# Kernel tuning notes

Measured on AMD Instinct MI355X. Metric: run time of the kernel, lower is better.

The kernel has to match this reference:

```python
import jax, jax.numpy as jnp
import numpy as np
from jax import lax

B, C, TX, TY = 16, 192, 512, 2048
SEG = 8192 // 256  # segment_frames = 32 (hop length 256)
NEG_INF = -1e9


def setup_inputs() -> dict:
    key = jax.random.key(0)
    ks = jax.random.split(key, 7)
    z = jax.random.normal(ks[0], (B, C, TY), jnp.float32)
    z_p = jax.random.normal(ks[1], (B, C, TY), jnp.float32)
    m_p = jax.random.normal(ks[2], (B, C, TX), jnp.float32)
    logs_p = 0.1 * jax.random.normal(ks[3], (B, C, TX), jnp.float32)
    x_lengths = jax.random.randint(ks[4], (B,), TX // 2, TX + 1, jnp.int32)
    y_lengths = jax.random.randint(ks[5], (B,), TY // 2, TY + 1, jnp.int32)
    rand_u = jax.random.uniform(ks[6], (B,), jnp.float32)
    return dict(z=z, z_p=z_p, m_p=m_p, logs_p=logs_p,
                x_lengths=x_lengths, y_lengths=y_lengths, rand_u=rand_u)


def neg_cent_fn(z_p, m_p, logs_p):
    # sum_c -0.5 * exp(-2 logs)[c,tx] * (z_p[c,ty] - m_p[c,tx])^2 - sum_c logs[c,tx]
    # expanded (z-m)^2 = z^2 - 2 z m + m^2 -> batched GEMMs (same math as broadcast form)
    s = jnp.exp(-2.0 * logs_p)                                 # [B,C,Tx]
    a = jnp.einsum('bct,bcs->bts', -0.5 * z_p * z_p, s)        # [B,Ty,Tx]
    b = jnp.einsum('bct,bcs->bts', z_p, s * m_p)               # [B,Ty,Tx]
    c = jnp.sum(-0.5 * s * m_p * m_p - logs_p, axis=1)         # [B,Tx]
    return a + b + c[:, None, :]


def maximum_path_single(value, t_x, t_y):
    # Monotonic alignment search DP on value [Ty,Tx], valid region [:t_y,:t_x].
    Ty, Tx = value.shape
    tx = jnp.arange(Tx)

    def fwd(v, row):
        v_shift = jnp.concatenate([jnp.full((1,), NEG_INF, v.dtype), v[:-1]])
        dirn = v_shift > v                      # True: best predecessor is tx-1
        v_new = row + jnp.maximum(v, v_shift)
        v_new = jnp.where(tx < t_x, v_new, NEG_INF)
        v_new = jnp.maximum(v_new, NEG_INF)     # clamp accumulation
        return v_new, dirn

    v0 = jnp.where(tx == 0, 0.0, NEG_INF)
    _, dirs = lax.scan(fwd, v0, value)          # dirs [Ty,Tx] bool

    def bwd(idx, j):
        active = j < t_y
        idx = jnp.where(j == t_y - 1, t_x - 1, idx)
        row = jnp.where(active, jnp.zeros((Tx,), value.dtype).at[idx].set(1.0), 0.0)
        idx = jnp.where(active, idx - dirs[j, idx].astype(idx.dtype), idx)
        return idx, row

    _, path_rev = lax.scan(bwd, jnp.int32(0), jnp.arange(Ty - 1, -1, -1))
    return path_rev[::-1]                       # [Ty,Tx] 0/1 path


def rand_slice_segments(z, y_lengths, rand_u):
    t = z.shape[2]
    safe = jnp.minimum(y_lengths, t)
    ids_max = jnp.maximum(safe - SEG, 0)
    ids = (rand_u * (ids_max.astype(jnp.float32) + 1e-8)).astype(jnp.int32)
    zs = jax.vmap(lambda zi, s: lax.dynamic_slice_in_dim(zi, s, SEG, axis=1))(z, ids)
    valid = (jnp.arange(SEG)[None, None, :] < (safe - ids)[:, None, None])
    return zs * valid.astype(z.dtype), ids


def reference(z, z_p, m_p, logs_p, x_lengths, y_lengths, rand_u):
    neg_cent = neg_cent_fn(z_p, m_p, logs_p)                     # [B,Ty,Tx]
    attn = jax.vmap(maximum_path_single)(neg_cent, x_lengths, y_lengths)
    attn = lax.stop_gradient(attn)                               # torch: no_grad + detach
    m_p_a = jnp.einsum('bts,bcs->bct', attn, m_p)                # [B,C,Ty]
    logs_p_a = jnp.einsum('bts,bcs->bct', attn, logs_p)          # [B,C,Ty]
    z_slice, ids_slice = rand_slice_segments(z, y_lengths, rand_u)
    return z_slice, ids_slice, attn, m_p_a, logs_p_a
```

## Files before the change

kernel.cpp:

```cpp
#include <hip/hip_runtime.h>
#include <stdint.h>

#define B_   16
#define C_   192
#define TX_  512
#define TY_  2048
#define K_   384
#define SEG_ 32
#define NEG_INF_ (-1e9f)


__global__ __launch_bounds__(128) void k_prep(const float* __restrict__ mp,
                                              const float* __restrict__ logsp,
                                              float* __restrict__ Bmat,
                                              float* __restrict__ cterm) {
    int b  = blockIdx.y;
    int tx = blockIdx.x * 128 + threadIdx.x;
    const float* mb = mp    + (size_t)b * C_ * TX_ + tx;
    const float* lb = logsp + (size_t)b * C_ * TX_ + tx;
    float* B0 = Bmat + (size_t)b * K_ * TX_ + tx;
    float acc = 0.f;
    for (int c = 0; c < C_; ++c) {
        float lg = lb[(size_t)c * TX_];
        float m  = mb[(size_t)c * TX_];
        float s  = expf(-2.f * lg);
        B0[(size_t)c * TX_]        = s;
        B0[(size_t)(C_ + c) * TX_] = s * m;
        acc += -0.5f * s * m * m - lg;
    }
    cterm[b * TX_ + tx] = acc;
}

__global__ __launch_bounds__(256) void k_gemm(const float* __restrict__ zp,
                                              const float* __restrict__ Bmat,
                                              const float* __restrict__ cterm,
                                              float* __restrict__ ncout) {
    __shared__ float As[16][128];
    __shared__ float Bs[16][128];
    int b  = blockIdx.z;
    int m0 = blockIdx.y * 128;
    int n0 = blockIdx.x * 128;
    int tid = threadIdx.x;
    int tm = tid >> 4;
    int tn = tid & 15;
    const float* zpb = zp   + (size_t)b * C_ * TY_;
    const float* Bb  = Bmat + (size_t)b * K_ * TX_;

    float acc[8][8];
#pragma unroll
    for (int i = 0; i < 8; ++i)
#pragma unroll
        for (int j = 0; j < 8; ++j) acc[i][j] = 0.f;

    int lrow = tid >> 5;
    int lcol = (tid & 31) << 2;

    for (int k0 = 0; k0 < K_; k0 += 16) {
        int ksrc = (k0 < C_) ? k0 : (k0 - C_);
        const float* Ab = zpb + (size_t)(ksrc + lrow) * TY_ + m0 + lcol;
        float4 z0 = *(const float4*)Ab;
        float4 z1 = *(const float4*)(Ab + (size_t)8 * TY_);
        if (k0 < C_) {
            z0.x = -0.5f * z0.x * z0.x; z0.y = -0.5f * z0.y * z0.y;
            z0.z = -0.5f * z0.z * z0.z; z0.w = -0.5f * z0.w * z0.w;
            z1.x = -0.5f * z1.x * z1.x; z1.y = -0.5f * z1.y * z1.y;
            z1.z = -0.5f * z1.z * z1.z; z1.w = -0.5f * z1.w * z1.w;
        }
        const float* Bp = Bb + (size_t)(k0 + lrow) * TX_ + n0 + lcol;
        float4 w0 = *(const float4*)Bp;
        float4 w1 = *(const float4*)(Bp + (size_t)8 * TX_);

        __syncthreads();
        *(float4*)&As[lrow][lcol]     = z0;
        *(float4*)&As[lrow + 8][lcol] = z1;
        *(float4*)&Bs[lrow][lcol]     = w0;
        *(float4*)&Bs[lrow + 8][lcol] = w1;
        __syncthreads();

#pragma unroll
        for (int kk = 0; kk < 16; ++kk) {
            float4 a0 = *(const float4*)&As[kk][tm * 8];
            float4 a1 = *(const float4*)&As[kk][tm * 8 + 4];
            float4 b0 = *(const float4*)&Bs[kk][tn * 8];
            float4 b1 = *(const float4*)&Bs[kk][tn * 8 + 4];
            float a[8]  = {a0.x, a0.y, a0.z, a0.w, a1.x, a1.y, a1.z, a1.w};
            float bb[8] = {b0.x, b0.y, b0.z, b0.w, b1.x, b1.y, b1.z, b1.w};
#pragma unroll
            for (int i = 0; i < 8; ++i)
#pragma unroll
                for (int j = 0; j < 8; ++j)
                    acc[i][j] = fmaf(a[i], bb[j], acc[i][j]);
        }
    }

    float cadd[8];
#pragma unroll
    for (int j = 0; j < 8; ++j) cadd[j] = cterm[b * TX_ + n0 + tn * 8 + j];

#pragma unroll
    for (int i = 0; i < 8; ++i) {
        int row = m0 + tm * 8 + i;
        float* orow = ncout + ((size_t)b * TY_ + row) * TX_ + n0 + tn * 8;
        float4 o0, o1;
        o0.x = acc[i][0] + cadd[0]; o0.y = acc[i][1] + cadd[1];
        o0.z = acc[i][2] + cadd[2]; o0.w = acc[i][3] + cadd[3];
        o1.x = acc[i][4] + cadd[4]; o1.y = acc[i][5] + cadd[5];
        o1.z = acc[i][6] + cadd[6]; o1.w = acc[i][7] + cadd[7];
        *(float4*)orow       = o0;
        *(float4*)(orow + 4) = o1;
    }
}

#define LOADG(g, P0, P1)                                                     \
    {                                                                        \
        const float* rp = base + (size_t)(g) * 8 * TX_;                      \
        _Pragma("unroll") for (int r = 0; r < 8; ++r) {                      \
            P0[r] = *(const float4*)(rp + (size_t)r * TX_);                  \
            P1[r] = *(const float4*)(rp + (size_t)r * TX_ + 4);              \
        }                                                                    \
    }

#define PROCG(g, P0, P1)                                                     \
    {                                                                        \
        unsigned dw0 = 0u, dw1 = 0u;                                         \
        _Pragma("unroll") for (int r = 0; r < 8; ++r) {                      \
            float rc[8] = {P0[r].x, P0[r].y, P0[r].z, P0[r].w,               \
                           P1[r].x, P1[r].y, P1[r].z, P1[r].w};              \
            float left = __shfl_up(v[7], 1);                                 \
            if (lane == 0) left = NEG_INF_;                                  \
            unsigned by = 0u;                                                \
            _Pragma("unroll") for (int k = 7; k >= 0; --k) {                 \
                float vs = (k == 0) ? left : v[k - 1];                       \
                if (vs > v[k]) by |= (1u << k);                              \
                v[k] = fmaxf(v[k], vs) + rc[k];                              \
            }                                                                \
            if (r < 4) dw0 |= by << (8 * r);                                 \
            else       dw1 |= by << (8 * (r - 4));                           \
        }                                                                    \
        sdirs32[((g) * 2) * 64 + lane]     = dw0;                            \
        sdirs32[((g) * 2 + 1) * 64 + lane] = dw1;                            \
    }

__global__ __launch_bounds__(64, 1) void k_dp(const float* __restrict__ nc,
                                              const int* __restrict__ xl,
                                              const int* __restrict__ yl,
                                              int* __restrict__ path) {
    extern __shared__ unsigned char sdirs[];
    unsigned* sdirs32 = (unsigned*)sdirs;
    int b    = blockIdx.x;
    int lane = threadIdx.x;
    int t_x  = xl[b];
    int t_y  = yl[b]; if (t_y > TY_) t_y = TY_;
    const float* base = nc + (size_t)b * TY_ * TX_ + lane * 8;

    int col0 = lane * 8;
    float v[8];
#pragma unroll
    for (int k = 0; k < 8; ++k) v[k] = (col0 + k == 0) ? 0.f : NEG_INF_;

    float4 c0[8], c1[8], n0[8], n1[8];
    int ng = (t_y + 7) >> 3;

    LOADG(0, c0, c1);
    for (int g = 0; g < ng; g += 2) {
        if (g + 1 < ng) LOADG(g + 1, n0, n1);
        __builtin_amdgcn_sched_barrier(0);
        PROCG(g, c0, c1);
        if (g + 1 < ng) {
            if (g + 2 < ng) LOADG(g + 2, c0, c1);
            __builtin_amdgcn_sched_barrier(0);
            PROCG(g + 1, n0, n1);
        }
    }

    __syncthreads();

    int* pb = path + b * TY_;
    for (int j = t_y + lane; j < TY_; j += 64) pb[j] = -1;

    if (lane == 0) {
        int idx = t_x - 1;
        int j   = t_y - 1;
        while (j >= 0) {
            int n  = (j + 1 < 8) ? (j + 1) : 8;
            int bs = (idx - 7) >> 3; if (bs < 0) bs = 0;
            int b2 = bs + 1;         if (b2 > 63) b2 = 63;
            unsigned lo[8], hi[8];
#pragma unroll
            for (int r = 0; r < 8; ++r) {
                if (r < n) {
                    int jr = j - r;
                    int rb = (jr >> 2) * 256 + (jr & 3);
                    lo[r] = sdirs[rb + bs * 4];
                    hi[r] = sdirs[rb + b2 * 4];
                }
            }
#pragma unroll
            for (int r = 0; r < 8; ++r) {
                if (r < n) {
                    pb[j - r] = idx;
                    int Bi = idx >> 3;
                    unsigned byte = (Bi == bs) ? lo[r] : hi[r];
                    idx -= (int)((byte >> (idx & 7)) & 1u);
                }
            }
            j -= n;
        }
    }
}

__global__ __launch_bounds__(256) void k_attn(const int* __restrict__ path,
                                              float* __restrict__ attn) {
    int i   = blockIdx.x * 256 + threadIdx.x;
    int tx0 = (i & 127) << 2;
    int bty = i >> 7;
    int p   = path[bty];
    float4 o;
    o.x = (p == tx0)     ? 1.f : 0.f;
    o.y = (p == tx0 + 1) ? 1.f : 0.f;
    o.z = (p == tx0 + 2) ? 1.f : 0.f;
    o.w = (p == tx0 + 3) ? 1.f : 0.f;
    ((float4*)attn)[i] = o;
}

__global__ __launch_bounds__(256) void k_proj(const int* __restrict__ path,
                                              const float* __restrict__ mp,
                                              const float* __restrict__ logsp,
                                              float* __restrict__ mpa,
                                              float* __restrict__ logsa) {
    int i   = blockIdx.x * 256 + threadIdx.x;
    int ty0 = (i & 511) << 2;
    int bc  = i >> 9;
    int b   = bc / C_;
    const int4 p4 = *(const int4*)(path + b * TY_ + ty0);
    const float* mrow = mp    + (size_t)bc * TX_;
    const float* lrow = logsp + (size_t)bc * TX_;
    float4 mo, lo;
    mo.x = (p4.x >= 0) ? mrow[p4.x] : 0.f;  lo.x = (p4.x >= 0) ? lrow[p4.x] : 0.f;
    mo.y = (p4.y >= 0) ? mrow[p4.y] : 0.f;  lo.y = (p4.y >= 0) ? lrow[p4.y] : 0.f;
    mo.z = (p4.z >= 0) ? mrow[p4.z] : 0.f;  lo.z = (p4.z >= 0) ? lrow[p4.z] : 0.f;
    mo.w = (p4.w >= 0) ? mrow[p4.w] : 0.f;  lo.w = (p4.w >= 0) ? lrow[p4.w] : 0.f;
    ((float4*)mpa)[i]   = mo;
    ((float4*)logsa)[i] = lo;
}

__global__ __launch_bounds__(256) void k_slice(const float* __restrict__ z,
                                               const int* __restrict__ yl,
                                               const float* __restrict__ ru,
                                               float* __restrict__ zs,
                                               float* __restrict__ oid) {
    int b = blockIdx.x;
    int safe = yl[b]; if (safe > TY_) safe = TY_;
    int idsmax = safe - SEG_; if (idsmax < 0) idsmax = 0;
    int ids = (int)(ru[b] * ((float)idsmax + 1e-8f));
    int lim = safe - ids;
    for (int t = threadIdx.x; t < C_ * SEG_; t += 256) {
        int c = t >> 5, k = t & 31;
        zs[b * C_ * SEG_ + t] =
            (k < lim) ? z[((size_t)b * C_ + c) * TY_ + ids + k] : 0.f;
    }
    if (threadIdx.x == 0) oid[b] = (float)ids;
}

extern "C" void kernel_launch(void* const* d_in, const int* in_sizes, int n_in,
                              void* d_out, int out_size, void* d_ws, size_t ws_size,
                              hipStream_t stream) {
    const float* z     = (const float*)d_in[0];
    const float* zp    = (const float*)d_in[1];
    const float* mp    = (const float*)d_in[2];
    const float* logsp = (const float*)d_in[3];
    const int*   xl    = (const int*)d_in[4];
    const int*   yl    = (const int*)d_in[5];
    const float* ru    = (const float*)d_in[6];

    float* out     = (float*)d_out;
    float* o_zs    = out;
    float* o_ids   = out + 98304;
    float* o_attn  = out + 98320;
    float* o_mpa   = out + 16875536;
    float* o_logsa = out + 23166992;

    float* Bmat  = (float*)d_ws;
    float* cterm = Bmat + (size_t)B_ * K_ * TX_;
    int*   path  = (int*)(cterm + B_ * TX_);

    hipFuncSetAttribute((const void*)k_dp,
                        hipFuncAttributeMaxDynamicSharedMemorySize,
                        TY_ * 64);

    hipLaunchKernelGGL(k_prep, dim3(TX_ / 128, B_), dim3(128), 0, stream,
                       mp, logsp, Bmat, cterm);
    hipLaunchKernelGGL(k_gemm, dim3(TX_ / 128, TY_ / 128, B_), dim3(256), 0, stream,
                       zp, Bmat, cterm, o_attn);
    hipLaunchKernelGGL(k_dp, dim3(B_), dim3(64), TY_ * 64, stream,
                       o_attn, xl, yl, path);
    hipLaunchKernelGGL(k_attn, dim3(B_ * TY_ * TX_ / 4 / 256), dim3(256), 0, stream,
                       path, o_attn);
    hipLaunchKernelGGL(k_proj, dim3(B_ * C_ * TY_ / 4 / 256), dim3(256), 0, stream,
                       path, mp, logsp, o_mpa, o_logsa);
    hipLaunchKernelGGL(k_slice, dim3(B_), dim3(256), 0, stream,
                       z, yl, ru, o_zs, o_ids);
}
```

Baseline: 778.6 us.

## Stream DP rows through LDS with async global_load_lds triple buffering

```diff
diff --git a/kernel.cpp b/kernel.cpp
--- a/kernel.cpp
+++ b/kernel.cpp
@@ -111,21 +111,28 @@
     }
 }
 
-#define LOADG(g, P0, P1)                                                     \
+#define WAITVM8() __builtin_amdgcn_s_waitcnt(3960)
+#define WAITVM0() __builtin_amdgcn_s_waitcnt(3952)
+
+#define ISSUE4(g)                                                            \
     {                                                                        \
-        const float* rp = base + (size_t)(g) * 8 * TX_;                      \
-        _Pragma("unroll") for (int r = 0; r < 8; ++r) {                      \
-            P0[r] = *(const float4*)(rp + (size_t)r * TX_);                  \
-            P1[r] = *(const float4*)(rp + (size_t)r * TX_ + 4);              \
-        }                                                                    \
-    }
-
-#define PROCG(g, P0, P1)                                                     \
+        const char* gp = base4 + (size_t)(g) * 8192 + lane * 16;             \
+        char* lp = (char*)stage + ((g) % 3) * 8192;                          \
+        _Pragma("unroll") for (int c = 0; c < 8; ++c)                        \
+            __builtin_amdgcn_global_load_lds(                                \
+                (const __attribute__((address_space(1))) void*)(gp + c * 1024), \
+                (__attribute__((address_space(3))) void*)(lp + c * 1024),    \
+                16, 0, 0);                                                   \
+    }
+
+#define PROCG4(g)                                                            \
     {                                                                        \
-        unsigned dw0 = 0u, dw1 = 0u;                                         \
-        _Pragma("unroll") for (int r = 0; r < 8; ++r) {                      \
-            float rc[8] = {P0[r].x, P0[r].y, P0[r].z, P0[r].w,               \
-                           P1[r].x, P1[r].y, P1[r].z, P1[r].w};              \
+        const float* rowp = (const float*)(stage + ((g) % 3) * 8192);        \
+        unsigned dw = 0u;                                                    \
+        _Pragma("unroll") for (int r = 0; r < 4; ++r) {                      \
+            float4 p0 = *(const float4*)(rowp + r * 512 + lane * 8);         \
+            float4 p1 = *(const float4*)(rowp + r * 512 + lane * 8 + 4);     \
+            float rc[8] = {p0.x, p0.y, p0.z, p0.w, p1.x, p1.y, p1.z, p1.w};  \
             float left = __shfl_up(v[7], 1);                                 \
             if (lane == 0) left = NEG_INF_;                                  \
             unsigned by = 0u;                                                \
@@ -134,11 +141,9 @@
                 if (vs > v[k]) by |= (1u << k);                              \
                 v[k] = fmaxf(v[k], vs) + rc[k];                              \
             }                                                                \
-            if (r < 4) dw0 |= by << (8 * r);                                 \
-            else       dw1 |= by << (8 * (r - 4));                           \
+            dw |= by << (8 * r);                                             \
         }                                                                    \
-        sdirs32[((g) * 2) * 64 + lane]     = dw0;                            \
-        sdirs32[((g) * 2 + 1) * 64 + lane] = dw1;                            \
+        sdirs32[(g) * 64 + lane] = dw;                                       \
     }
 
 __global__ __launch_bounds__(64, 1) void k_dp(const float* __restrict__ nc,
@@ -146,32 +151,32 @@
                                               const int* __restrict__ yl,
                                               int* __restrict__ path) {
     extern __shared__ unsigned char sdirs[];
-    unsigned* sdirs32 = (unsigned*)sdirs;
+    unsigned* sdirs32    = (unsigned*)sdirs;
+    unsigned char* stage = sdirs + 131072;
     int b    = blockIdx.x;
     int lane = threadIdx.x;
     int t_x  = xl[b];
     int t_y  = yl[b]; if (t_y > TY_) t_y = TY_;
-    const float* base = nc + (size_t)b * TY_ * TX_ + lane * 8;
+    const char* base4 = (const char*)(nc + (size_t)b * TY_ * TX_);
 
     int col0 = lane * 8;
     float v[8];
 #pragma unroll
     for (int k = 0; k < 8; ++k) v[k] = (col0 + k == 0) ? 0.f : NEG_INF_;
 
-    float4 c0[8], c1[8], n0[8], n1[8];
-    int ng = (t_y + 7) >> 3;
-
-    LOADG(0, c0, c1);
-    for (int g = 0; g < ng; g += 2) {
-        if (g + 1 < ng) LOADG(g + 1, n0, n1);
+    int ng = (t_y + 3) >> 2;
+
+    ISSUE4(0);
+    ISSUE4(1);
+    for (int g = 0; g < ng - 1; ++g) {
+        WAITVM8();
         __builtin_amdgcn_sched_barrier(0);
-        PROCG(g, c0, c1);
-        if (g + 1 < ng) {
-            if (g + 2 < ng) LOADG(g + 2, c0, c1);
-            __builtin_amdgcn_sched_barrier(0);
-            PROCG(g + 1, n0, n1);
-        }
-    }
+        PROCG4(g);
+        if (g + 2 < ng) ISSUE4(g + 2);
+    }
+    WAITVM0();
+    __builtin_amdgcn_sched_barrier(0);
+    PROCG4(ng - 1);
 
     __syncthreads();
 
@@ -286,13 +291,13 @@
 
     hipFuncSetAttribute((const void*)k_dp,
                         hipFuncAttributeMaxDynamicSharedMemorySize,
-                        TY_ * 64);
+                        131072 + 3 * 8192);
 
     hipLaunchKernelGGL(k_prep, dim3(TX_ / 128, B_), dim3(128), 0, stream,
                        mp, logsp, Bmat, cterm);
     hipLaunchKernelGGL(k_gemm, dim3(TX_ / 128, TY_ / 128, B_), dim3(256), 0, stream,
                        zp, Bmat, cterm, o_attn);
-    hipLaunchKernelGGL(k_dp, dim3(B_), dim3(64), TY_ * 64, stream,
+    hipLaunchKernelGGL(k_dp, dim3(B_), dim3(64), 131072 + 3 * 8192, stream,
                        o_attn, xl, yl, path);
     hipLaunchKernelGGL(k_attn, dim3(B_ * TY_ * TX_ / 4 / 256), dim3(256), 0, stream,
                        path, o_attn);
```

After: 936.3 us. 20.3% more time.

## Warp-specialize DP kernel with producer waves staging rows through LDS ring

Applied to the files above, without the earlier changes.

```diff
diff --git a/kernel.cpp b/kernel.cpp
--- a/kernel.cpp
+++ b/kernel.cpp
@@ -111,69 +111,91 @@
     }
 }
 
-#define LOADG(g, P0, P1)                                                     \
-    {                                                                        \
-        const float* rp = base + (size_t)(g) * 8 * TX_;                      \
-        _Pragma("unroll") for (int r = 0; r < 8; ++r) {                      \
-            P0[r] = *(const float4*)(rp + (size_t)r * TX_);                  \
-            P1[r] = *(const float4*)(rp + (size_t)r * TX_ + 4);              \
-        }                                                                    \
-    }
-
-#define PROCG(g, P0, P1)                                                     \
-    {                                                                        \
-        unsigned dw0 = 0u, dw1 = 0u;                                         \
-        _Pragma("unroll") for (int r = 0; r < 8; ++r) {                      \
-            float rc[8] = {P0[r].x, P0[r].y, P0[r].z, P0[r].w,               \
-                           P1[r].x, P1[r].y, P1[r].z, P1[r].w};              \
-            float left = __shfl_up(v[7], 1);                                 \
-            if (lane == 0) left = NEG_INF_;                                  \
-            unsigned by = 0u;                                                \
-            _Pragma("unroll") for (int k = 7; k >= 0; --k) {                 \
-                float vs = (k == 0) ? left : v[k - 1];                       \
-                if (vs > v[k]) by |= (1u << k);                              \
-                v[k] = fmaxf(v[k], vs) + rc[k];                              \
-            }                                                                \
-            if (r < 4) dw0 |= by << (8 * r);                                 \
-            else       dw1 |= by << (8 * (r - 4));                           \
-        }                                                                    \
-        sdirs32[((g) * 2) * 64 + lane]     = dw0;                            \
-        sdirs32[((g) * 2 + 1) * 64 + lane] = dw1;                            \
-    }
-
-__global__ __launch_bounds__(64, 1) void k_dp(const float* __restrict__ nc,
-                                              const int* __restrict__ xl,
-                                              const int* __restrict__ yl,
-                                              int* __restrict__ path) {
+#define NSLOT_ 3
+
+__global__ __launch_bounds__(256, 1) void k_dp(const float* __restrict__ nc,
+                                               const int* __restrict__ xl,
+                                               const int* __restrict__ yl,
+                                               int* __restrict__ path) {
     extern __shared__ unsigned char sdirs[];
     unsigned* sdirs32 = (unsigned*)sdirs;
+    float*    stagef  = (float*)(sdirs + 131072);
+    unsigned* flags   = (unsigned*)(sdirs + 131072 + NSLOT_ * 8192);
+    unsigned* cons_ctr = flags + NSLOT_;
+
     int b    = blockIdx.x;
-    int lane = threadIdx.x;
+    int tid  = threadIdx.x;
+    int w    = tid >> 6;
+    int lane = tid & 63;
     int t_x  = xl[b];
     int t_y  = yl[b]; if (t_y > TY_) t_y = TY_;
-    const float* base = nc + (size_t)b * TY_ * TX_ + lane * 8;
+    const float* ncb = nc + (size_t)b * TY_ * TX_;
+    int ng = (t_y + 3) >> 2;
+
+    if (tid < NSLOT_ + 1) flags[tid] = 0;
+    __syncthreads();
+
+    if (w != 0) {
+        int a0off = ((lane & 1) * 256 + (lane >> 1) * 4);
+        for (int g = w - 1; g < ng; g += 3) {
+            while ((int)__hip_atomic_load(cons_ctr, __ATOMIC_ACQUIRE,
+                                          __HIP_MEMORY_SCOPE_WORKGROUP) < g - 2) {}
+            int j0 = g * 4;
+            const float4* r0 = (const float4*)(ncb + (size_t)(j0    ) * TX_);
+            const float4* r1 = (const float4*)(ncb + (size_t)(j0 + 1) * TX_);
+            const float4* r2 = (const float4*)(ncb + (size_t)(j0 + 2) * TX_);
+            const float4* r3 = (const float4*)(ncb + (size_t)(j0 + 3) * TX_);
+            float4 q00 = r0[lane], q01 = r0[64 + lane];
+            float4 q10 = r1[lane], q11 = r1[64 + lane];
+            float4 q20 = r2[lane], q21 = r2[64 + lane];
+            float4 q30 = r3[lane], q31 = r3[64 + lane];
+            float* sb = stagef + (g % NSLOT_) * 2048;
+            *(float4*)(sb             + a0off)       = q00;
+            *(float4*)(sb             + a0off + 128) = q01;
+            *(float4*)(sb + 512       + a0off)       = q10;
+            *(float4*)(sb + 512       + a0off + 128) = q11;
+            *(float4*)(sb + 1024      + a0off)       = q20;
+            *(float4*)(sb + 1024      + a0off + 128) = q21;
+            *(float4*)(sb + 1536      + a0off)       = q30;
+            *(float4*)(sb + 1536      + a0off + 128) = q31;
+            if (lane == 0)
+                __hip_atomic_store(&flags[g % NSLOT_], (unsigned)(g + 1),
+                                   __ATOMIC_RELEASE, __HIP_MEMORY_SCOPE_WORKGROUP);
+        }
+        return;
+    }
 
     int col0 = lane * 8;
     float v[8];
 #pragma unroll
     for (int k = 0; k < 8; ++k) v[k] = (col0 + k == 0) ? 0.f : NEG_INF_;
 
-    float4 c0[8], c1[8], n0[8], n1[8];
-    int ng = (t_y + 7) >> 3;
-
-    LOADG(0, c0, c1);
-    for (int g = 0; g < ng; g += 2) {
-        if (g + 1 < ng) LOADG(g + 1, n0, n1);
-        __builtin_amdgcn_sched_barrier(0);
-        PROCG(g, c0, c1);
-        if (g + 1 < ng) {
-            if (g + 2 < ng) LOADG(g + 2, c0, c1);
-            __builtin_amdgcn_sched_barrier(0);
-            PROCG(g + 1, n0, n1);
-        }
-    }
-
-    __syncthreads();
+    for (int g = 0; g < ng; ++g) {
+        while (__hip_atomic_load(&flags[g % NSLOT_], __ATOMIC_ACQUIRE,
+                                 __HIP_MEMORY_SCOPE_WORKGROUP) != (unsigned)(g + 1)) {}
+        const float* rowp = stagef + (g % NSLOT_) * 2048;
+        unsigned dw = 0u;
+#pragma unroll
+        for (int r = 0; r < 4; ++r) {
+            float4 p0 = *(const float4*)(rowp + r * 512 + lane * 4);
+            float4 p1 = *(const float4*)(rowp + r * 512 + 256 + lane * 4);
+            float rc[8] = {p0.x, p0.y, p0.z, p0.w, p1.x, p1.y, p1.z, p1.w};
+            float left = __shfl_up(v[7], 1);
+            if (lane == 0) left = NEG_INF_;
+            unsigned by = 0u;
+#pragma unroll
+            for (int k = 7; k >= 0; --k) {
+                float vs = (k == 0) ? left : v[k - 1];
+                if (vs > v[k]) by |= (1u << k);
+                v[k] = fmaxf(v[k], vs) + rc[k];
+            }
+            dw |= by << (8 * r);
+        }
+        sdirs32[g * 64 + lane] = dw;
+        if (lane == 0)
+            __hip_atomic_store(cons_ctr, (unsigned)(g + 1),
+                               __ATOMIC_RELEASE, __HIP_MEMORY_SCOPE_WORKGROUP);
+    }
 
     int* pb = path + b * TY_;
     for (int j = t_y + lane; j < TY_; j += 64) pb[j] = -1;
@@ -284,15 +306,16 @@
     float* cterm = Bmat + (size_t)B_ * K_ * TX_;
     int*   path  = (int*)(cterm + B_ * TX_);
 
+    const int dp_lds = 131072 + NSLOT_ * 8192 + 64;
+
     hipFuncSetAttribute((const void*)k_dp,
-                        hipFuncAttributeMaxDynamicSharedMemorySize,
-                        TY_ * 64);
+                        hipFuncAttributeMaxDynamicSharedMemorySize, dp_lds);
 
     hipLaunchKernelGGL(k_prep, dim3(TX_ / 128, B_), dim3(128), 0, stream,
                        mp, logsp, Bmat, cterm);
     hipLaunchKernelGGL(k_gemm, dim3(TX_ / 128, TY_ / 128, B_), dim3(256), 0, stream,
                        zp, Bmat, cterm, o_attn);
-    hipLaunchKernelGGL(k_dp, dim3(B_), dim3(64), TY_ * 64, stream,
+    hipLaunchKernelGGL(k_dp, dim3(B_), dim3(256), dp_lds, stream,
                        o_attn, xl, yl, path);
     hipLaunchKernelGGL(k_attn, dim3(B_ * TY_ * TX_ / 4 / 256), dim3(256), 0, stream,
                        path, o_attn);
```

After: 854.5 us. +9.7%, slower.
